# Kernel tuning notes

Hardware: AMD Instinct MI355X
Metric: run time of the kernel (lower is better)

## Reference

```python
import jax, jax.numpy as jnp
import numpy as np
from math import factorial

L_MAX = 3
K = 256
N = 2048


def _cg_coeff(l1, m1, l2, m2, l3, m3):
    # Clebsch-Gordan coefficient <l1 m1 l2 m2 | l3 m3> via the Racah formula.
    if m3 != m1 + m2:
        return 0.0
    pref = ((2 * l3 + 1) * factorial(l3 + l1 - l2) * factorial(l3 - l1 + l2)
            * factorial(l1 + l2 - l3) / factorial(l1 + l2 + l3 + 1)) ** 0.5
    pref *= (factorial(l3 + m3) * factorial(l3 - m3) * factorial(l1 - m1)
             * factorial(l1 + m1) * factorial(l2 - m2) * factorial(l2 + m2)) ** 0.5
    s = 0.0
    for k in range(0, l1 + l2 - l3 + 1):
        d = [k, l1 + l2 - l3 - k, l1 - m1 - k, l2 + m2 - k,
             l3 - l2 + m1 + k, l3 - l1 - m2 + k]
        if min(d) < 0:
            continue
        den = 1.0
        for x in d:
            den *= factorial(x)
        s += (-1.0) ** k / den
    return pref * s


def _cg_tensor(l1, l2, l3):
    out = np.zeros((2 * l1 + 1, 2 * l2 + 1, 2 * l3 + 1), dtype=np.float32)
    for m1 in range(-l1, l1 + 1):
        for m2 in range(-l2, l2 + 1):
            m3 = m1 + m2
            if -l3 <= m3 <= l3:
                out[m1 + l1, m2 + l2, m3 + l3] = _cg_coeff(l1, m1, l2, m2, l3, m3)
    return jnp.asarray(out)


# All (l1, l2) -> l coupling paths allowed by the triangle inequality, l <= L_MAX.
PATHS = {l: [(l1, l2) for l1 in range(L_MAX + 1) for l2 in range(L_MAX + 1)
             if abs(l1 - l2) <= l <= l1 + l2] for l in range(L_MAX + 1)}
CG = {(l1, l2, l): _cg_tensor(l1, l2, l)
      for l in range(L_MAX + 1) for (l1, l2) in PATHS[l]}


def _forward(f1, f2, U, W):
    outs = []
    for l in range(L_MAX + 1):
        # CG tensor product: elementwise over channels k, coupled over (m1, m2) -> m.
        parts = [jnp.einsum('abm,nak,nbk->nmk', CG[(l1, l2, l)], f1[l1], f2[l2])
                 for (l1, l2) in PATHS[l]]
        tp = jnp.concatenate(parts, axis=-1)          # [N, 2l+1, n_paths(l)*K]
        mixed = jnp.einsum('nmc,ck->nmk', tp, U[l])   # U_dict per-l mixing -> [N, 2l+1, K]
        mixed = jnp.einsum('nmk,kj->nmj', mixed, W[l])  # learned per-l linear
        outs.append(f1[l] + mixed)                    # residual
    return tuple(outs)


def setup_inputs() -> dict:
    key = jax.random.key(0)
    ks = jax.random.split(key, 16)
    inp = {}
    for l in range(L_MAX + 1):
        inp[f'f1_l{l}'] = jax.random.normal(ks[l], (N, 2 * l + 1, K), jnp.float32)
        inp[f'f2_l{l}'] = jax.random.normal(ks[4 + l], (N, 2 * l + 1, K), jnp.float32)
        cin = len(PATHS[l]) * K
        inp[f'U_{l}'] = jax.random.normal(ks[8 + l], (cin, K), jnp.float32) / float(np.sqrt(cin))
        inp[f'W_{l}'] = jax.random.normal(ks[12 + l], (K, K), jnp.float32) / float(np.sqrt(K))
    return inp


def reference(f1_l0, f1_l1, f1_l2, f1_l3,
              f2_l0, f2_l1, f2_l2, f2_l3,
              U_0, U_1, U_2, U_3,
              W_0, W_1, W_2, W_3):
    f1 = [f1_l0, f1_l1, f1_l2, f1_l3]
    f2 = [f2_l0, f2_l1, f2_l2, f2_l3]
    U = [U_0, U_1, U_2, U_3]
    W = [W_0, W_1, W_2, W_3]
    return _forward(f1, f2, U, W)
```

## Files before the change

### kernel.cpp

```cpp
#include <hip/hip_runtime.h>
#include <math.h>

typedef __attribute__((ext_vector_type(4))) float f32x4;
typedef __attribute__((ext_vector_type(2))) float f32x2;
typedef __attribute__((ext_vector_type(8))) __bf16 bf16x8;
typedef __attribute__((ext_vector_type(4))) __bf16 bf16x4;
typedef __attribute__((ext_vector_type(2))) __bf16 bf16x2;

__device__ __constant__ int GP_L[34]  = {0,0,0,0, 1,1,1,1,1,1,1,1,1, 2,2,2,2,2,2,2,2,2,2,2, 3,3,3,3,3,3,3,3,3,3};
__device__ __constant__ int GP_L1[34] = {0,1,2,3, 0,1,1,1,2,2,2,3,3, 0,1,1,1,2,2,2,2,3,3,3, 0,1,1,2,2,2,3,3,3,3};
__device__ __constant__ int GP_L2[34] = {0,1,2,3, 1,0,1,2,1,2,3,2,3, 2,1,2,3,0,1,2,3,1,2,3, 3,2,3,1,2,3,0,1,2,3};

__device__ double dfact(int n) { double r = 1.0; for (int i = 2; i <= n; ++i) r *= (double)i; return r; }

__device__ double cg_coeff(int l1, int m1, int l2, int m2, int l3, int m3) {
  if (m3 != m1 + m2) return 0.0;
  double pref = sqrt((2.0 * l3 + 1.0) * dfact(l3 + l1 - l2) * dfact(l3 - l1 + l2)
                     * dfact(l1 + l2 - l3) / dfact(l1 + l2 + l3 + 1));
  pref *= sqrt(dfact(l3 + m3) * dfact(l3 - m3) * dfact(l1 - m1) * dfact(l1 + m1)
               * dfact(l2 - m2) * dfact(l2 + m2));
  double s = 0.0;
  for (int k = 0; k <= l1 + l2 - l3; ++k) {
    int d0 = k, d1 = l1 + l2 - l3 - k, d2 = l1 - m1 - k, d3 = l2 + m2 - k;
    int d4 = l3 - l2 + m1 + k, d5 = l3 - l1 - m2 + k;
    if (d0 < 0 || d1 < 0 || d2 < 0 || d3 < 0 || d4 < 0 || d5 < 0) continue;
    double den = dfact(d0) * dfact(d1) * dfact(d2) * dfact(d3) * dfact(d4) * dfact(d5);
    s += ((k & 1) ? -1.0 : 1.0) / den;
  }
  return pref * s;
}

__global__ __launch_bounds__(256) void prep(
    const float* __restrict__ u0, const float* __restrict__ u1,
    const float* __restrict__ u2, const float* __restrict__ u3,
    const float* __restrict__ w0, const float* __restrict__ w1,
    const float* __restrict__ w2, const float* __restrict__ w3,
    __bf16* __restrict__ Ubf, __bf16* __restrict__ Wt, float* __restrict__ cg) {
  const int bid = blockIdx.x, tid = threadIdx.x;
  if (bid < 2176) {
    long i = (long)bid * 256 + tid;
    const long b1 = 65536, b2 = 212992, b3 = 393216;
    const float* src; long s;
    if (i < b1)      { src = u0; s = i; }
    else if (i < b2) { src = u1; s = i - b1; }
    else if (i < b3) { src = u2; s = i - b2; }
    else             { src = u3; s = i - b3; }
    float4 v = ((const float4*)src)[s];
    bf16x4 o;
    o[0] = (__bf16)v.x; o[1] = (__bf16)v.y; o[2] = (__bf16)v.z; o[3] = (__bf16)v.w;
    ((bf16x4*)Ubf)[i] = o;
  } else if (bid < 3200) {
    int b = bid - 2176;
    int l = b >> 8, j = b & 255;
    const float* W = (l == 0) ? w0 : (l == 1) ? w1 : (l == 2) ? w2 : w3;
    Wt[((long)l << 16) + (j << 8) + tid] = (__bf16)W[(tid << 8) + j];
  } else {
    int idx = (bid - 3200) * 256 + tid;
    if (idx < 34 * 49) {
      int gp = idx / 49, r = idx % 49;
      int m1i = r / 7, m2i = r % 7;
      int l3 = GP_L[gp], l1 = GP_L1[gp], l2 = GP_L2[gp];
      float v = 0.f;
      if (m1i <= 2 * l1 && m2i <= 2 * l2) {
        int m1 = m1i - l1, m2 = m2i - l2, m3 = m1 + m2;
        if (m3 >= -l3 && m3 <= l3) v = (float)cg_coeff(l1, m1, l2, m2, l3, m3);
      }
      cg[idx] = v;
    }
  }
}

struct GemmDesc {
  const __bf16* A[4];
  const __bf16* B[4];
  void*         C[4];
  int start[4];
  int lmap[4];
  int Kd[4];
  int Nc[4];
};

__device__ __forceinline__ void gload_lds16(const void* g, void* l) {
  __builtin_amdgcn_global_load_lds((const __attribute__((address_space(1))) void*)g,
                                   (__attribute__((address_space(3))) void*)l, 16, 0, 0);
}

__global__ __launch_bounds__(256) void gemm_batched(GemmDesc d) {
  __shared__ __bf16 As[128 * 64];
  __shared__ __bf16 Bs[128 * 64];
  const int tid = threadIdx.x;
  const int bid = blockIdx.x;
  int seg = 0;
  if (bid >= d.start[1]) seg = 1;
  if (bid >= d.start[2]) seg = 2;
  if (bid >= d.start[3]) seg = 3;
  const int l = d.lmap[seg];
  const int rel = bid - d.start[seg];
  const int Kd = d.Kd[l], Nc = d.Nc[l];
  const int nTN = Nc >> 7;
  const int tM = rel / nTN, tN = rel % nTN;

  const int lane = tid & 63, wave = tid >> 6;
  const int wm = (wave >> 1) << 6, wn = (wave & 1) << 6;
  const int lr = lane & 15, lk = (lane >> 4) << 3;

  f32x4 acc[4][4] = {};

  const int r32 = tid >> 3;
  const int sl = ((tid & 7) ^ (r32 & 7)) << 3;
  const __bf16* Ag = d.A[l] + (long)(tM * 128 + r32) * Kd + sl;
  const __bf16* Bg = d.B[l] + (long)(tN * 128 + r32) * Kd + sl;
  char* AsB = (char*)As;
  char* BsB = (char*)Bs;

  for (int kt = 0; kt < Kd; kt += 64) {
#pragma unroll
    for (int i = 0; i < 4; ++i) {
      gload_lds16(Ag + (long)i * 32 * Kd + kt, AsB + i * 4096 + tid * 16);
      gload_lds16(Bg + (long)i * 32 * Kd + kt, BsB + i * 4096 + tid * 16);
    }
    __syncthreads();

#pragma unroll
    for (int kk = 0; kk < 64; kk += 32) {
      bf16x8 af[4], bfr[4];
#pragma unroll
      for (int mi = 0; mi < 4; ++mi)
        af[mi] = *(const bf16x8*)(AsB + ((wm + mi * 16 + lr) << 7)
                                      + ((((kk + lk) << 1)) ^ ((lr & 7) << 4)));
#pragma unroll
      for (int ni = 0; ni < 4; ++ni)
        bfr[ni] = *(const bf16x8*)(BsB + ((wn + ni * 16 + lr) << 7)
                                       + ((((kk + lk) << 1)) ^ ((lr & 7) << 4)));
#pragma unroll
      for (int mi = 0; mi < 4; ++mi)
#pragma unroll
        for (int ni = 0; ni < 4; ++ni)
          acc[mi][ni] = __builtin_amdgcn_mfma_f32_16x16x32_bf16(af[mi], bfr[ni], acc[mi][ni], 0, 0, 0);
    }
    __syncthreads();
  }

  const long col0 = (long)tN * 128 + wn + lr;
  const long row0 = (long)tM * 128 + wm + ((lane >> 4) << 2);
#pragma unroll
  for (int mi = 0; mi < 4; ++mi) {
#pragma unroll
    for (int j = 0; j < 4; ++j) {
      long r = row0 + mi * 16 + j;
      long base = r * (long)Nc + col0;
#pragma unroll
      for (int ni = 0; ni < 4; ++ni)
        ((__bf16*)d.C[l])[base + ni * 16] = (__bf16)acc[mi][ni][j];
    }
  }
}

#define TPW2(LV, DST, CIN, GOFF, P, L1V, L2V)                                    \
  { f32x2 tp[2 * (LV) + 1];                                                      \
    _Pragma("unroll") for (int m = 0; m <= 2 * (LV); ++m) { tp[m][0] = 0.f; tp[m][1] = 0.f; } \
    const float* cgt = cg + ((GOFF) + (P)) * 49;                                 \
    _Pragma("unroll") for (int a = 0; a <= 2 * (L1V); ++a)                       \
      _Pragma("unroll") for (int b = 0; b <= 2 * (L2V); ++b) {                   \
        const int m = a + b - ((L1V) + (L2V) - (LV));                            \
        if (m >= 0 && m <= 2 * (LV)) {                                           \
          float c = cgt[a * 7 + b];                                              \
          tp[m][0] = fmaf(c, v1[CUM[L1V] + a][0] * v2[CUM[L2V] + b][0], tp[m][0]); \
          tp[m][1] = fmaf(c, v1[CUM[L1V] + a][1] * v2[CUM[L2V] + b][1], tp[m][1]); \
        } }                                                                      \
    __bf16* o = (DST) + (n * (2 * (LV) + 1)) * (CIN) + (P) * 256 + k2;           \
    _Pragma("unroll") for (int m = 0; m <= 2 * (LV); ++m) {                      \
      bf16x2 ov; ov[0] = (__bf16)tp[m][0]; ov[1] = (__bf16)tp[m][1];             \
      *(bf16x2*)(o + (long)m * (CIN)) = ov; } }

template <int LMASK>
__global__ __launch_bounds__(256) void tp_all(
    const float* __restrict__ f10, const float* __restrict__ f11,
    const float* __restrict__ f12, const float* __restrict__ f13,
    const float* __restrict__ f20, const float* __restrict__ f21,
    const float* __restrict__ f22, const float* __restrict__ f23,
    const float* __restrict__ cg,
    __bf16* __restrict__ A0, __bf16* __restrict__ A1,
    __bf16* __restrict__ A2, __bf16* __restrict__ A3) {
  const int tid = threadIdx.x;
  const long n = (long)blockIdx.x * 2 + (tid >> 7);
  const int k2 = (tid & 127) << 1;
  constexpr int CUM[4] = {0, 1, 4, 9};
  const float* f1s[4] = {f10, f11, f12, f13};
  const float* f2s[4] = {f20, f21, f22, f23};

  f32x2 v1[16], v2[16];
#pragma unroll
  for (int l1 = 0; l1 < 4; ++l1) {
    const float* p1 = f1s[l1] + (n * (2 * l1 + 1)) * 256 + k2;
    const float* p2 = f2s[l1] + (n * (2 * l1 + 1)) * 256 + k2;
#pragma unroll
    for (int a = 0; a <= 2 * l1; ++a) {
      v1[CUM[l1] + a] = *(const f32x2*)(p1 + (long)a * 256);
      v2[CUM[l1] + a] = *(const f32x2*)(p2 + (long)a * 256);
    }
  }

  if constexpr (LMASK & 1) {
    TPW2(0, A0, 1024, 0, 0, 0, 0)  TPW2(0, A0, 1024, 0, 1, 1, 1)
    TPW2(0, A0, 1024, 0, 2, 2, 2)  TPW2(0, A0, 1024, 0, 3, 3, 3)
  }
  if constexpr (LMASK & 2) {
    TPW2(1, A1, 2304, 4, 0, 0, 1)  TPW2(1, A1, 2304, 4, 1, 1, 0)
    TPW2(1, A1, 2304, 4, 2, 1, 1)  TPW2(1, A1, 2304, 4, 3, 1, 2)
    TPW2(1, A1, 2304, 4, 4, 2, 1)  TPW2(1, A1, 2304, 4, 5, 2, 2)
    TPW2(1, A1, 2304, 4, 6, 2, 3)  TPW2(1, A1, 2304, 4, 7, 3, 2)
    TPW2(1, A1, 2304, 4, 8, 3, 3)
  }
  if constexpr (LMASK & 4) {
    TPW2(2, A2, 2816, 13, 0, 0, 2)  TPW2(2, A2, 2816, 13, 1, 1, 1)
    TPW2(2, A2, 2816, 13, 2, 1, 2)  TPW2(2, A2, 2816, 13, 3, 1, 3)
    TPW2(2, A2, 2816, 13, 4, 2, 0)  TPW2(2, A2, 2816, 13, 5, 2, 1)
    TPW2(2, A2, 2816, 13, 6, 2, 2)  TPW2(2, A2, 2816, 13, 7, 2, 3)
    TPW2(2, A2, 2816, 13, 8, 3, 1)  TPW2(2, A2, 2816, 13, 9, 3, 2)
    TPW2(2, A2, 2816, 13, 10, 3, 3)
  }
  if constexpr (LMASK & 8) {
    TPW2(3, A3, 2560, 24, 0, 0, 3)  TPW2(3, A3, 2560, 24, 1, 1, 2)
    TPW2(3, A3, 2560, 24, 2, 1, 3)  TPW2(3, A3, 2560, 24, 3, 2, 1)
    TPW2(3, A3, 2560, 24, 4, 2, 2)  TPW2(3, A3, 2560, 24, 5, 2, 3)
    TPW2(3, A3, 2560, 24, 6, 3, 0)  TPW2(3, A3, 2560, 24, 7, 3, 1)
    TPW2(3, A3, 2560, 24, 8, 3, 2)  TPW2(3, A3, 2560, 24, 9, 3, 3)
  }
}

struct MainDesc {
  const __bf16* A[4];
  const __bf16* B[4];
  float*        C[4];
  const float*  R[4];
  int start[4];
  int lmap[4];
  int cin4[4];
};

__global__ __launch_bounds__(512) void gemm_main(MainDesc d) {
  __shared__ __align__(16) char sm[98304];
  const int tid = threadIdx.x;
  int bid;
  {
    const int cpx = gridDim.x >> 3;
    bid = (blockIdx.x & 7) * cpx + (blockIdx.x >> 3);
  }
  int seg = 0;
  if (bid >= d.start[1]) seg = 1;
  if (bid >= d.start[2]) seg = 2;
  if (bid >= d.start[3]) seg = 3;
  const int l = d.lmap[seg];
  const int tM = bid - d.start[seg];
  const int cin = d.cin4[l];
  const int NT = cin >> 6;

  const __bf16* __restrict__ Aseg = d.A[l] + (long)tM * 128 * cin;
  const __bf16* __restrict__ Bseg = d.B[l];

  const int srow = tid >> 3;
  const int sx = ((tid & 7) ^ (srow & 7)) << 3;

  f32x4 acc[4][4] = {};

  const int lane = tid & 63, wave = tid >> 6;
  const int wm = (wave >> 2) << 6;
  const int wn = (wave & 3) << 6;
  const int lr = lane & 15, lkb = (lane >> 4) << 3;

#pragma unroll
  for (int i = 0; i < 2; ++i)
    gload_lds16(Aseg + (long)(i * 64 + srow) * cin + sx, sm + i * 8192 + tid * 16);
#pragma unroll
  for (int i = 0; i < 4; ++i)
    gload_lds16(Bseg + (long)(i * 64 + srow) * cin + sx, sm + 32768 + i * 8192 + tid * 16);
  __syncthreads();

  for (int t = 0; t < NT; ++t) {
    const int cur = t & 1;
    if (t + 1 < NT) {
      const int ktn = (t + 1) << 6;
      char* An = sm + (cur ^ 1) * 16384;
      char* Bn = sm + 32768 + (cur ^ 1) * 32768;
#pragma unroll
      for (int i = 0; i < 2; ++i)
        gload_lds16(Aseg + (long)(i * 64 + srow) * cin + ktn + sx, An + i * 8192 + tid * 16);
#pragma unroll
      for (int i = 0; i < 4; ++i)
        gload_lds16(Bseg + (long)(i * 64 + srow) * cin + ktn + sx, Bn + i * 8192 + tid * 16);
    }
    const char* Ab = sm + cur * 16384;
    const char* Bb = sm + 32768 + cur * 32768;
#pragma unroll
    for (int kk = 0; kk < 64; kk += 32) {
      bf16x8 af[4], bfr[4];
#pragma unroll
      for (int mi = 0; mi < 4; ++mi) {
        const int row = wm + mi * 16 + lr;
        af[mi] = *(const bf16x8*)(Ab + row * 128 + ((((kk + lkb) << 1)) ^ ((row & 7) << 4)));
      }
#pragma unroll
      for (int ni = 0; ni < 4; ++ni) {
        const int row = wn + ni * 16 + lr;
        bfr[ni] = *(const bf16x8*)(Bb + row * 128 + ((((kk + lkb) << 1)) ^ ((row & 7) << 4)));
      }
#pragma unroll
      for (int mi = 0; mi < 4; ++mi)
#pragma unroll
        for (int ni = 0; ni < 4; ++ni)
          acc[mi][ni] = __builtin_amdgcn_mfma_f32_16x16x32_bf16(af[mi], bfr[ni], acc[mi][ni], 0, 0, 0);
    }
    __syncthreads();
  }

  float* __restrict__ Cout = d.C[l];
  const float* __restrict__ Resid = d.R[l];
  const int col0 = wn + lr;
  const int rb = (lane >> 4) << 2;
#pragma unroll
  for (int mi = 0; mi < 4; ++mi)
#pragma unroll
    for (int j = 0; j < 4; ++j) {
      const long row = (long)tM * 128 + wm + mi * 16 + rb + j;
      const long base = row * 256 + col0;
#pragma unroll
      for (int ni = 0; ni < 4; ++ni)
        Cout[base + ni * 16] = acc[mi][ni][j] + Resid[base + ni * 16];
    }
}

extern "C" void kernel_launch(void* const* d_in, const int* in_sizes, int n_in,
                              void* d_out, int out_size, void* d_ws, size_t ws_size,
                              hipStream_t stream) {
  const float* F1[4], * F2[4], * Uin[4], * Win[4];
  for (int l = 0; l < 4; ++l) {
    F1[l]  = (const float*)d_in[4 * l + 0];
    F2[l]  = (const float*)d_in[4 * l + 1];
    Uin[l] = (const float*)d_in[4 * l + 2];
    Win[l] = (const float*)d_in[4 * l + 3];
  }
  static const int  cin_[4]  = {1024, 2304, 2816, 2560};
  static const int  cum_[4]  = {0, 1024, 3328, 6144};
  static const long moff_[4] = {0, 524288, 2097152, 4718592};
  static const int  nTM_[4]  = {16, 48, 80, 112};
  static const long asz_[4]  = {4194304L, 28311552L, 57671680L, 73400320L};

  char* ws = (char*)d_ws;
  float*  cg   = (float*)ws;
  __bf16* Ubf  = (__bf16*)(ws + 8192);
  __bf16* Wtbf = (__bf16*)(ws + 8192 + 4456448);
  __bf16* UWt  = (__bf16*)(ws + 5242880);
  const long ABASE = 10485760;
  const bool big = ws_size >= (size_t)(ABASE + asz_[0] + asz_[1] + asz_[2] + asz_[3]);

  __bf16* Ab[4];
  if (big) {
    long off = ABASE;
    for (int l = 0; l < 4; ++l) { Ab[l] = (__bf16*)(ws + off); off += asz_[l]; }
  } else {
    for (int l = 0; l < 4; ++l) Ab[l] = (__bf16*)(ws + ABASE);
  }

  hipLaunchKernelGGL(prep, dim3(3207), dim3(256), 0, stream,
                     Uin[0], Uin[1], Uin[2], Uin[3],
                     Win[0], Win[1], Win[2], Win[3], Ubf, Wtbf, cg);

  {
    GemmDesc d;
    int starts[4] = {0, 40, 84, 120};
    int lmap[4]   = {3, 2, 1, 0};
    for (int s = 0; s < 4; ++s) { d.start[s] = starts[s]; d.lmap[s] = lmap[s]; }
    for (int l = 0; l < 4; ++l) {
      d.A[l] = Wtbf + (long)l * 65536;
      d.B[l] = Ubf + (long)cum_[l] * 256;
      d.C[l] = (void*)(UWt + (long)cum_[l] * 256);
      d.Kd[l] = 256;
      d.Nc[l] = cin_[l];
    }
    hipLaunchKernelGGL(gemm_batched, dim3(136), dim3(256), 0, stream, d);
  }

  if (big) {
    hipLaunchKernelGGL((tp_all<15>), dim3(1024), dim3(256), 0, stream,
                       F1[0], F1[1], F1[2], F1[3], F2[0], F2[1], F2[2], F2[3],
                       cg, Ab[0], Ab[1], Ab[2], Ab[3]);
    MainDesc d;
    int starts[4] = {0, 112, 192, 240};
    int lmap[4]   = {3, 2, 1, 0};
    for (int s = 0; s < 4; ++s) { d.start[s] = starts[s]; d.lmap[s] = lmap[s]; }
    for (int l = 0; l < 4; ++l) {
      d.A[l] = Ab[l];
      d.B[l] = UWt + (long)cum_[l] * 256;
      d.C[l] = (float*)d_out + moff_[l];
      d.R[l] = F1[l];
      d.cin4[l] = cin_[l];
    }
    hipLaunchKernelGGL(gemm_main, dim3(256), dim3(512), 0, stream, d);
  } else {
    for (int l = 0; l < 4; ++l) {
      switch (l) {
        case 0: hipLaunchKernelGGL((tp_all<1>), dim3(1024), dim3(256), 0, stream,
                  F1[0],F1[1],F1[2],F1[3], F2[0],F2[1],F2[2],F2[3], cg,
                  Ab[0],Ab[1],Ab[2],Ab[3]); break;
        case 1: hipLaunchKernelGGL((tp_all<2>), dim3(1024), dim3(256), 0, stream,
                  F1[0],F1[1],F1[2],F1[3], F2[0],F2[1],F2[2],F2[3], cg,
                  Ab[0],Ab[1],Ab[2],Ab[3]); break;
        case 2: hipLaunchKernelGGL((tp_all<4>), dim3(1024), dim3(256), 0, stream,
                  F1[0],F1[1],F1[2],F1[3], F2[0],F2[1],F2[2],F2[3], cg,
                  Ab[0],Ab[1],Ab[2],Ab[3]); break;
        case 3: hipLaunchKernelGGL((tp_all<8>), dim3(1024), dim3(256), 0, stream,
                  F1[0],F1[1],F1[2],F1[3], F2[0],F2[1],F2[2],F2[3], cg,
                  Ab[0],Ab[1],Ab[2],Ab[3]); break;
      }
      MainDesc d;
      for (int s = 0; s < 4; ++s) {
        d.start[s] = (s == 0) ? 0 : 0x7fffffff;
        d.lmap[s] = l;
      }
      for (int ll = 0; ll < 4; ++ll) {
        d.A[ll] = Ab[l];
        d.B[ll] = UWt + (long)cum_[l] * 256;
        d.C[ll] = (float*)d_out + moff_[l];
        d.R[ll] = F1[l];
        d.cin4[ll] = cin_[l];
      }
      hipLaunchKernelGGL(gemm_main, dim3(nTM_[l]), dim3(512), 0, stream, d);
    }
  }
  (void)in_sizes; (void)n_in; (void)out_size; (void)ws_size;
}
```

Measured before the change: 135.2 us.

## Fuse UW precompute GEMM into TP kernel and triple-buffer main GEMM

The small U·W bf16 GEMM is merged into the tensor-product kernel as extra blocks, so the two independent stages share one launch and can overlap. The main GEMM moves from 512 to 256 threads per block, each wave computing a 64x128 tile. It gains a three-stage LDS pipeline with explicit vmcnt waits, raw barriers and setprio around the MFMA loop. The aim is to hide global-load latency and drop a launch, at the cost of 144KB of LDS per block and fewer waves per CU.

```diff
diff --git a/kernel.cpp b/kernel.cpp
--- a/kernel.cpp
+++ b/kernel.cpp
@@ -73,7 +73,7 @@
 struct GemmDesc {
   const __bf16* A[4];
   const __bf16* B[4];
-  void*         C[4];
+  __bf16*       C[4];
   int start[4];
   int lmap[4];
   int Kd[4];
@@ -85,11 +85,8 @@
                                    (__attribute__((address_space(3))) void*)l, 16, 0, 0);
 }
 
-__global__ __launch_bounds__(256) void gemm_batched(GemmDesc d) {
-  __shared__ __bf16 As[128 * 64];
-  __shared__ __bf16 Bs[128 * 64];
+__device__ void uw_body(const GemmDesc& d, int bid, char* sm) {
   const int tid = threadIdx.x;
-  const int bid = blockIdx.x;
   int seg = 0;
   if (bid >= d.start[1]) seg = 1;
   if (bid >= d.start[2]) seg = 2;
@@ -110,8 +107,8 @@
   const int sl = ((tid & 7) ^ (r32 & 7)) << 3;
   const __bf16* Ag = d.A[l] + (long)(tM * 128 + r32) * Kd + sl;
   const __bf16* Bg = d.B[l] + (long)(tN * 128 + r32) * Kd + sl;
-  char* AsB = (char*)As;
-  char* BsB = (char*)Bs;
+  char* AsB = sm;
+  char* BsB = sm + 16384;
 
   for (int kt = 0; kt < Kd; kt += 64) {
 #pragma unroll
@@ -123,20 +120,20 @@
 
 #pragma unroll
     for (int kk = 0; kk < 64; kk += 32) {
-      bf16x8 af[4], bfr[4];
+      bf16x8 af[4], bq[4];
 #pragma unroll
       for (int mi = 0; mi < 4; ++mi)
         af[mi] = *(const bf16x8*)(AsB + ((wm + mi * 16 + lr) << 7)
                                       + ((((kk + lk) << 1)) ^ ((lr & 7) << 4)));
 #pragma unroll
       for (int ni = 0; ni < 4; ++ni)
-        bfr[ni] = *(const bf16x8*)(BsB + ((wn + ni * 16 + lr) << 7)
-                                       + ((((kk + lk) << 1)) ^ ((lr & 7) << 4)));
+        bq[ni] = *(const bf16x8*)(BsB + ((wn + ni * 16 + lr) << 7)
+                                      + ((((kk + lk) << 1)) ^ ((lr & 7) << 4)));
 #pragma unroll
       for (int mi = 0; mi < 4; ++mi)
 #pragma unroll
         for (int ni = 0; ni < 4; ++ni)
-          acc[mi][ni] = __builtin_amdgcn_mfma_f32_16x16x32_bf16(af[mi], bfr[ni], acc[mi][ni], 0, 0, 0);
+          acc[mi][ni] = __builtin_amdgcn_mfma_f32_16x16x32_bf16(af[mi], bq[ni], acc[mi][ni], 0, 0, 0);
     }
     __syncthreads();
   }
@@ -144,16 +141,15 @@
   const long col0 = (long)tN * 128 + wn + lr;
   const long row0 = (long)tM * 128 + wm + ((lane >> 4) << 2);
 #pragma unroll
-  for (int mi = 0; mi < 4; ++mi) {
+  for (int mi = 0; mi < 4; ++mi)
 #pragma unroll
     for (int j = 0; j < 4; ++j) {
       long r = row0 + mi * 16 + j;
       long base = r * (long)Nc + col0;
 #pragma unroll
       for (int ni = 0; ni < 4; ++ni)
-        ((__bf16*)d.C[l])[base + ni * 16] = (__bf16)acc[mi][ni][j];
-    }
-  }
+        d.C[l][base + ni * 16] = (__bf16)acc[mi][ni][j];
+    }
 }
 
 #define TPW2(LV, DST, CIN, GOFF, P, L1V, L2V)                                    \
@@ -174,16 +170,16 @@
       *(bf16x2*)(o + (long)m * (CIN)) = ov; } }
 
 template <int LMASK>
-__global__ __launch_bounds__(256) void tp_all(
+__device__ void tp_body(
     const float* __restrict__ f10, const float* __restrict__ f11,
     const float* __restrict__ f12, const float* __restrict__ f13,
     const float* __restrict__ f20, const float* __restrict__ f21,
     const float* __restrict__ f22, const float* __restrict__ f23,
     const float* __restrict__ cg,
     __bf16* __restrict__ A0, __bf16* __restrict__ A1,
-    __bf16* __restrict__ A2, __bf16* __restrict__ A3) {
+    __bf16* __restrict__ A2, __bf16* __restrict__ A3, int bid) {
   const int tid = threadIdx.x;
-  const long n = (long)blockIdx.x * 2 + (tid >> 7);
+  const long n = (long)bid * 2 + (tid >> 7);
   const int k2 = (tid & 127) << 1;
   constexpr int CUM[4] = {0, 1, 4, 9};
   const float* f1s[4] = {f10, f11, f12, f13};
@@ -226,6 +222,26 @@
     TPW2(3, A3, 2560, 24, 4, 2, 2)  TPW2(3, A3, 2560, 24, 5, 2, 3)
     TPW2(3, A3, 2560, 24, 6, 3, 0)  TPW2(3, A3, 2560, 24, 7, 3, 1)
     TPW2(3, A3, 2560, 24, 8, 3, 2)  TPW2(3, A3, 2560, 24, 9, 3, 3)
+  }
+}
+
+template <int LMASK>
+__global__ __launch_bounds__(256) void tp_uw(
+    const float* __restrict__ f10, const float* __restrict__ f11,
+    const float* __restrict__ f12, const float* __restrict__ f13,
+    const float* __restrict__ f20, const float* __restrict__ f21,
+    const float* __restrict__ f22, const float* __restrict__ f23,
+    const float* __restrict__ cg,
+    __bf16* __restrict__ A0, __bf16* __restrict__ A1,
+    __bf16* __restrict__ A2, __bf16* __restrict__ A3,
+    GemmDesc gd, int nUW) {
+  __shared__ __align__(16) char sm[32768];
+  const int bid = (int)blockIdx.x;
+  if (bid < nUW) {
+    uw_body(gd, bid, sm);
+  } else if constexpr (LMASK != 0) {
+    tp_body<LMASK>(f10, f11, f12, f13, f20, f21, f22, f23, cg,
+                   A0, A1, A2, A3, bid - nUW);
   }
 }
 
@@ -239,13 +255,13 @@
   int cin4[4];
 };
 
-__global__ __launch_bounds__(512) void gemm_main(MainDesc d) {
-  __shared__ __align__(16) char sm[98304];
+__global__ __launch_bounds__(256) void gemm_main(MainDesc d) {
+  __shared__ __align__(16) char sm[147456];
   const int tid = threadIdx.x;
   int bid;
   {
     const int cpx = gridDim.x >> 3;
-    bid = (blockIdx.x & 7) * cpx + (blockIdx.x >> 3);
+    bid = ((int)blockIdx.x & 7) * cpx + ((int)blockIdx.x >> 3);
   }
   int seg = 0;
   if (bid >= d.start[1]) seg = 1;
@@ -262,70 +278,79 @@
   const int srow = tid >> 3;
   const int sx = ((tid & 7) ^ (srow & 7)) << 3;
 
-  f32x4 acc[4][4] = {};
-
   const int lane = tid & 63, wave = tid >> 6;
-  const int wm = (wave >> 2) << 6;
-  const int wn = (wave & 3) << 6;
+  const int wm = (wave >> 1) << 6;
+  const int wn = (wave & 1) << 7;
   const int lr = lane & 15, lkb = (lane >> 4) << 3;
 
-#pragma unroll
-  for (int i = 0; i < 2; ++i)
-    gload_lds16(Aseg + (long)(i * 64 + srow) * cin + sx, sm + i * 8192 + tid * 16);
+  f32x4 acc[4][8];
 #pragma unroll
   for (int i = 0; i < 4; ++i)
-    gload_lds16(Bseg + (long)(i * 64 + srow) * cin + sx, sm + 32768 + i * 8192 + tid * 16);
-  __syncthreads();
+#pragma unroll
+    for (int j = 0; j < 8; ++j) { acc[i][j][0]=0.f; acc[i][j][1]=0.f; acc[i][j][2]=0.f; acc[i][j][3]=0.f; }
+
+#define STAGE(s, t)                                                              \
+  { char* base_ = sm + (s) * 49152;                                              \
+    const long kt_ = (long)(t) << 6;                                             \
+    _Pragma("unroll")                                                            \
+    for (int i = 0; i < 4; ++i)                                                  \
+      gload_lds16(Aseg + (long)(i * 32 + srow) * cin + kt_ + sx,                 \
+                  base_ + i * 4096 + tid * 16);                                  \
+    _Pragma("unroll")                                                            \
+    for (int i = 0; i < 8; ++i)                                                  \
+      gload_lds16(Bseg + (long)(i * 32 + srow) * cin + kt_ + sx,                 \
+                  base_ + 16384 + i * 4096 + tid * 16); }
+
+  STAGE(0, 0)
+  STAGE(1, 1)
 
   for (int t = 0; t < NT; ++t) {
-    const int cur = t & 1;
-    if (t + 1 < NT) {
-      const int ktn = (t + 1) << 6;
-      char* An = sm + (cur ^ 1) * 16384;
-      char* Bn = sm + 32768 + (cur ^ 1) * 32768;
-#pragma unroll
-      for (int i = 0; i < 2; ++i)
-        gload_lds16(Aseg + (long)(i * 64 + srow) * cin + ktn + sx, An + i * 8192 + tid * 16);
-#pragma unroll
-      for (int i = 0; i < 4; ++i)
-        gload_lds16(Bseg + (long)(i * 64 + srow) * cin + ktn + sx, Bn + i * 8192 + tid * 16);
-    }
-    const char* Ab = sm + cur * 16384;
-    const char* Bb = sm + 32768 + cur * 32768;
+    if (t + 2 < NT) STAGE((t + 2) % 3, t + 2)
+    if (t + 3 <= NT)      asm volatile("s_waitcnt vmcnt(24)" ::: "memory");
+    else if (t + 2 == NT) asm volatile("s_waitcnt vmcnt(12)" ::: "memory");
+    else                  asm volatile("s_waitcnt vmcnt(0)"  ::: "memory");
+    __builtin_amdgcn_s_barrier();
+    __builtin_amdgcn_sched_barrier(0);
+
+    const char* Ab = sm + (t % 3) * 49152;
+    const char* Bb = Ab + 16384;
+    __builtin_amdgcn_s_setprio(1);
 #pragma unroll
     for (int kk = 0; kk < 64; kk += 32) {
-      bf16x8 af[4], bfr[4];
+      bf16x8 af[4], bq[8];
 #pragma unroll
       for (int mi = 0; mi < 4; ++mi) {
         const int row = wm + mi * 16 + lr;
         af[mi] = *(const bf16x8*)(Ab + row * 128 + ((((kk + lkb) << 1)) ^ ((row & 7) << 4)));
       }
 #pragma unroll
-      for (int ni = 0; ni < 4; ++ni) {
+      for (int ni = 0; ni < 8; ++ni) {
         const int row = wn + ni * 16 + lr;
-        bfr[ni] = *(const bf16x8*)(Bb + row * 128 + ((((kk + lkb) << 1)) ^ ((row & 7) << 4)));
+        bq[ni] = *(const bf16x8*)(Bb + row * 128 + ((((kk + lkb) << 1)) ^ ((row & 7) << 4)));
       }
 #pragma unroll
       for (int mi = 0; mi < 4; ++mi)
 #pragma unroll
-        for (int ni = 0; ni < 4; ++ni)
-          acc[mi][ni] = __builtin_amdgcn_mfma_f32_16x16x32_bf16(af[mi], bfr[ni], acc[mi][ni], 0, 0, 0);
-    }
-    __syncthreads();
-  }
+        for (int ni = 0; ni < 8; ++ni)
+          acc[mi][ni] = __builtin_amdgcn_mfma_f32_16x16x32_bf16(af[mi], bq[ni], acc[mi][ni], 0, 0, 0);
+    }
+    __builtin_amdgcn_s_setprio(0);
+    __builtin_amdgcn_sched_barrier(0);
+    __builtin_amdgcn_s_barrier();
+  }
+#undef STAGE
 
   float* __restrict__ Cout = d.C[l];
   const float* __restrict__ Resid = d.R[l];
-  const int col0 = wn + lr;
   const int rb = (lane >> 4) << 2;
 #pragma unroll
   for (int mi = 0; mi < 4; ++mi)
 #pragma unroll
     for (int j = 0; j < 4; ++j) {
       const long row = (long)tM * 128 + wm + mi * 16 + rb + j;
-      const long base = row * 256 + col0;
-#pragma unroll
-      for (int ni = 0; ni < 4; ++ni)
+      const long base = row * 256 + wn + lr;
+#pragma unroll
+      for (int ni = 0; ni < 8; ++ni)
         Cout[base + ni * 16] = acc[mi][ni][j] + Resid[base + ni * 16];
     }
 }
@@ -366,25 +391,24 @@
                      Uin[0], Uin[1], Uin[2], Uin[3],
                      Win[0], Win[1], Win[2], Win[3], Ubf, Wtbf, cg);
 
+  GemmDesc gd;
   {
-    GemmDesc d;
     int starts[4] = {0, 40, 84, 120};
     int lmap[4]   = {3, 2, 1, 0};
-    for (int s = 0; s < 4; ++s) { d.start[s] = starts[s]; d.lmap[s] = lmap[s]; }
+    for (int s = 0; s < 4; ++s) { gd.start[s] = starts[s]; gd.lmap[s] = lmap[s]; }
     for (int l = 0; l < 4; ++l) {
-      d.A[l] = Wtbf + (long)l * 65536;
-      d.B[l] = Ubf + (long)cum_[l] * 256;
-      d.C[l] = (void*)(UWt + (long)cum_[l] * 256);
-      d.Kd[l] = 256;
-      d.Nc[l] = cin_[l];
-    }
-    hipLaunchKernelGGL(gemm_batched, dim3(136), dim3(256), 0, stream, d);
+      gd.A[l] = Wtbf + (long)l * 65536;
+      gd.B[l] = Ubf + (long)cum_[l] * 256;
+      gd.C[l] = UWt + (long)cum_[l] * 256;
+      gd.Kd[l] = 256;
+      gd.Nc[l] = cin_[l];
+    }
   }
 
   if (big) {
-    hipLaunchKernelGGL((tp_all<15>), dim3(1024), dim3(256), 0, stream,
+    hipLaunchKernelGGL((tp_uw<15>), dim3(1160), dim3(256), 0, stream,
                        F1[0], F1[1], F1[2], F1[3], F2[0], F2[1], F2[2], F2[3],
-                       cg, Ab[0], Ab[1], Ab[2], Ab[3]);
+                       cg, Ab[0], Ab[1], Ab[2], Ab[3], gd, 136);
     MainDesc d;
     int starts[4] = {0, 112, 192, 240};
     int lmap[4]   = {3, 2, 1, 0};
@@ -396,22 +420,25 @@
       d.R[l] = F1[l];
       d.cin4[l] = cin_[l];
     }
-    hipLaunchKernelGGL(gemm_main, dim3(256), dim3(512), 0, stream, d);
+    hipLaunchKernelGGL(gemm_main, dim3(256), dim3(256), 0, stream, d);
   } else {
+    hipLaunchKernelGGL((tp_uw<0>), dim3(136), dim3(256), 0, stream,
+                       F1[0], F1[1], F1[2], F1[3], F2[0], F2[1], F2[2], F2[3],
+                       cg, Ab[0], Ab[1], Ab[2], Ab[3], gd, 136);
     for (int l = 0; l < 4; ++l) {
       switch (l) {
-        case 0: hipLaunchKernelGGL((tp_all<1>), dim3(1024), dim3(256), 0, stream,
+        case 0: hipLaunchKernelGGL((tp_uw<1>), dim3(1024), dim3(256), 0, stream,
                   F1[0],F1[1],F1[2],F1[3], F2[0],F2[1],F2[2],F2[3], cg,
-                  Ab[0],Ab[1],Ab[2],Ab[3]); break;
-        case 1: hipLaunchKernelGGL((tp_all<2>), dim3(1024), dim3(256), 0, stream,
+                  Ab[0],Ab[1],Ab[2],Ab[3], gd, 0); break;
+        case 1: hipLaunchKernelGGL((tp_uw<2>), dim3(1024), dim3(256), 0, stream,
                   F1[0],F1[1],F1[2],F1[3], F2[0],F2[1],F2[2],F2[3], cg,
-                  Ab[0],Ab[1],Ab[2],Ab[3]); break;
-        case 2: hipLaunchKernelGGL((tp_all<4>), dim3(1024), dim3(256), 0, stream,
+                  Ab[0],Ab[1],Ab[2],Ab[3], gd, 0); break;
+        case 2: hipLaunchKernelGGL((tp_uw<4>), dim3(1024), dim3(256), 0, stream,
                   F1[0],F1[1],F1[2],F1[3], F2[0],F2[1],F2[2],F2[3], cg,
-                  Ab[0],Ab[1],Ab[2],Ab[3]); break;
-        case 3: hipLaunchKernelGGL((tp_all<8>), dim3(1024), dim3(256), 0, stream,
+                  Ab[0],Ab[1],Ab[2],Ab[3], gd, 0); break;
+        case 3: hipLaunchKernelGGL((tp_uw<8>), dim3(1024), dim3(256), 0, stream,
                   F1[0],F1[1],F1[2],F1[3], F2[0],F2[1],F2[2],F2[3], cg,
-                  Ab[0],Ab[1],Ab[2],Ab[3]); break;
+                  Ab[0],Ab[1],Ab[2],Ab[3], gd, 0); break;
       }
       MainDesc d;
       for (int s = 0; s < 4; ++s) {
@@ -425,7 +452,7 @@
         d.R[ll] = F1[l];
         d.cin4[ll] = cin_[l];
       }
-      hipLaunchKernelGGL(gemm_main, dim3(nTM_[l]), dim3(512), 0, stream, d);
+      hipLaunchKernelGGL(gemm_main, dim3(nTM_[l]), dim3(256), 0, stream, d);
     }
   }
   (void)in_sizes; (void)n_in; (void)out_size; (void)ws_size;
```

Measured after the change: 149.5 us. 10.6% more time.
